# Kernel tuning notes

Hardware: AMD Instinct MI355X
Metric: run time of the kernel (lower is better)

The kernel has to match this reference:

```python
import jax, jax.numpy as jnp
import numpy as np

B, S, D = 16, 2048, 1024
FF = 4 * D
ST, EN = 0, 512          # target_dims['start'], target_dims['end']
DT = EN - ST             # intervened subspace dim


def setup_inputs() -> dict:
    key = jax.random.key(0)
    k = jax.random.split(key, 6)
    hidden_states = jax.random.normal(k[0], (B, S, D), dtype=jnp.float32)
    eot_indices = jax.random.randint(k[1], (B,), 0, S)
    scale = 0.02
    W1 = jax.random.normal(k[2], (D, FF), dtype=jnp.float32) * scale
    W2 = jax.random.normal(k[3], (FF, D), dtype=jnp.float32) * scale
    W_rot = jax.random.normal(k[4], (DT, DT), dtype=jnp.float32) * scale
    W_inv = jax.random.normal(k[5], (DT, DT), dtype=jnp.float32) * scale
    return {"hidden_states": hidden_states, "W1": W1, "W2": W2,
            "W_rot": W_rot, "W_inv": W_inv, "eot_indices": eot_indices}


def reference(hidden_states, W1, W2, W_rot, W_inv, eot_indices):
    # layers[0]: transformer FFN block (stand-in for the wrapped encoder layer)
    h = jax.nn.gelu(hidden_states @ W1) @ W2          # [B, S, D]
    b = jnp.arange(h.shape[0])
    # LinearLayer branch: gather per-example eot row, slice target subspace
    rows = h[b, eot_indices]                          # [B, D]
    target = rows[:, ST:EN]                           # [B, DT]
    # LinearLayer -> InverseLinearLayer: rotate then un-rotate the subspace
    intervention = (target @ W_rot) @ W_inv           # [B, DT]
    # scatter/replace back into the flattened hidden states (vectorized form
    # of the per-example flatten/slice/cat/stack loop in the original code)
    new_rows = rows.at[:, ST:EN].set(intervention)    # [B, D]
    reps = h.at[b, eot_indices].set(new_rows)         # [B, S, D]
    return reps
```

## Files before the change

kernel.cpp:

```cpp
#include <hip/hip_runtime.h>
#include <hip/hip_bf16.h>
#include <stdint.h>

#define B_SZ  16
#define S_SZ  2048
#define D_SZ  1024
#define FF_SZ 4096
#define DT_SZ 512

typedef __bf16 bf16x8 __attribute__((ext_vector_type(8)));
typedef float  f32x4  __attribute__((ext_vector_type(4)));
typedef short  short8 __attribute__((ext_vector_type(8)));

__device__ __forceinline__ short f2bf(float x) {
    union { float f; uint32_t u; } v; v.f = x;
    uint32_t r = (v.u + 0x7fffu + ((v.u >> 16) & 1u)) >> 16;
    return (short)(uint16_t)r;
}

__global__ void cast_x_kernel(const float* __restrict__ src, short* __restrict__ dst, int n8) {
    int i = blockIdx.x * 256 + threadIdx.x;
    if (i >= n8) return;
    const float4* s4 = reinterpret_cast<const float4*>(src);
    float4 a = s4[2 * i], b = s4[2 * i + 1];
    short8 v;
    v[0] = f2bf(a.x); v[1] = f2bf(a.y); v[2] = f2bf(a.z); v[3] = f2bf(a.w);
    v[4] = f2bf(b.x); v[5] = f2bf(b.y); v[6] = f2bf(b.z); v[7] = f2bf(b.w);
    reinterpret_cast<short8*>(dst)[i] = v;
}

__global__ void transpose_cast_kernel(const float* __restrict__ src, short* __restrict__ dst,
                                      int R, int C) {
    __shared__ float tile[32][33];
    int c0 = blockIdx.x * 32, r0 = blockIdx.y * 32;
    int tx = threadIdx.x, ty = threadIdx.y;
#pragma unroll
    for (int i = 0; i < 32; i += 8)
        tile[ty + i][tx] = src[(size_t)(r0 + ty + i) * C + (c0 + tx)];
    __syncthreads();
#pragma unroll
    for (int i = 0; i < 32; i += 8)
        dst[(size_t)(c0 + ty + i) * R + (r0 + tx)] = f2bf(tile[tx][ty + i]);
}


#define GLOAD(srcp, dstofs)                                                   \
    __builtin_amdgcn_global_load_lds(                                         \
        (__attribute__((address_space(1))) void*)(srcp),                      \
        (__attribute__((address_space(3))) void*)(ldsb + (dstofs)), 16, 0, 0)

#define ABASE(S) ((S) * 65536)
#define BBASE(S) ((S) * 65536 + 32768)

#define STG_A(S, H, T) do {                                                                 \
    GLOAD(gA[H][0] + (size_t)(T) * 64, ABASE(S) + (H) * 16384 +        w * 1024);           \
    GLOAD(gA[H][1] + (size_t)(T) * 64, ABASE(S) + (H) * 16384 + 8192 + w * 1024);           \
} while (0)
#define STG_B(S, H, T) do {                                                                 \
    GLOAD(gB[H][0] + (size_t)(T) * 64, BBASE(S) + (H) * 16384 +        w * 1024);           \
    GLOAD(gB[H][1] + (size_t)(T) * 64, BBASE(S) + (H) * 16384 + 8192 + w * 1024);           \
} while (0)
#define NOSTG ((void)0)
#define VM2  asm volatile("s_waitcnt vmcnt(2)" ::: "memory")
#define VM0  asm volatile("s_waitcnt vmcnt(0)" ::: "memory")
#define NOVM ((void)0)

#define PHASE(S, KS, MIG, RB, VM, ...) do {                                                 \
    if (RB) {                                                                               \
        _Pragma("unroll")                                                                   \
        for (int ni = 0; ni < 4; ++ni)                                                      \
            bfv[ni] = *reinterpret_cast<const bf16x8*>(                                     \
                ldsb + BBASE(S) + (offB[ni] ^ ((KS) * 64)));                                \
    }                                                                                       \
    _Pragma("unroll")                                                                       \
    for (int mi = 0; mi < 4; ++mi)                                                          \
        af[mi] = *reinterpret_cast<const bf16x8*>(                                          \
            ldsb + ABASE(S) + (offA[(MIG) * 4 + mi] ^ ((KS) * 64)));                        \
    __VA_ARGS__;                                                                            \
    __builtin_amdgcn_s_barrier();                                                           \
    asm volatile("s_waitcnt lgkmcnt(0)" ::: "memory");                                      \
    __builtin_amdgcn_sched_barrier(0);                                                      \
    __builtin_amdgcn_s_setprio(1);                                                          \
    _Pragma("unroll")                                                                       \
    for (int mi = 0; mi < 4; ++mi)                                                          \
        _Pragma("unroll")                                                                   \
        for (int ni = 0; ni < 4; ++ni)                                                      \
            acc[(MIG) * 4 + mi][ni] = __builtin_amdgcn_mfma_f32_16x16x32_bf16(              \
                af[mi], bfv[ni], acc[(MIG) * 4 + mi][ni], 0, 0, 0);                         \
    __builtin_amdgcn_s_setprio(0);                                                          \
    __builtin_amdgcn_sched_barrier(0);                                                      \
    VM;                                                                                     \
    __builtin_amdgcn_s_barrier();                                                           \
} while (0)

#define ITER_FULL(T) do {                                                                   \
    PHASE(0, 0, 0, 1, NOVM, STG_B(1, 1, (T) + 1));                                          \
    PHASE(0, 0, 1, 0, NOVM, STG_A(1, 0, (T) + 1));                                          \
    PHASE(0, 1, 0, 1, NOVM, STG_A(1, 1, (T) + 1));                                          \
    PHASE(0, 1, 1, 0, VM2,  STG_B(0, 0, (T) + 2));                                          \
    PHASE(1, 0, 0, 1, NOVM, STG_B(0, 1, (T) + 2));                                          \
    PHASE(1, 0, 1, 0, NOVM, STG_A(0, 0, (T) + 2));                                          \
    PHASE(1, 1, 0, 1, NOVM, STG_A(0, 1, (T) + 2));                                          \
    PHASE(1, 1, 1, 0, VM2,  STG_B(1, 0, (T) + 3));                                          \
} while (0)

#define ITER_LAST(T) do {                                                                   \
    PHASE(0, 0, 0, 1, NOVM, STG_B(1, 1, (T) + 1));                                          \
    PHASE(0, 0, 1, 0, NOVM, STG_A(1, 0, (T) + 1));                                          \
    PHASE(0, 1, 0, 1, NOVM, STG_A(1, 1, (T) + 1));                                          \
    PHASE(0, 1, 1, 0, VM0,  NOSTG);                                                         \
    PHASE(1, 0, 0, 1, NOVM, NOSTG);                                                         \
    PHASE(1, 0, 1, 0, NOVM, NOSTG);                                                         \
    PHASE(1, 1, 0, 1, NOVM, NOSTG);                                                         \
    PHASE(1, 1, 1, 0, NOVM, NOSTG);                                                         \
} while (0)

template <bool GELU_BF16>
__global__ __launch_bounds__(512, 2)
void gemm256_kernel(const short* __restrict__ A, const short* __restrict__ Bt,
                    void* __restrict__ Cout, int M, int N, int K) {
    __shared__ char lds2[2][65536];
    char* ldsb = &lds2[0][0];

    const int tid = threadIdx.x;
    const int w   = tid >> 6;
    const int l   = tid & 63;
    const int wm  = w >> 2;
    const int wn  = w & 3;
    const int kq  = l >> 4;
    const int l15 = l & 15;

    const int nwg = gridDim.x;
    int swzw = blockIdx.x;
    if ((nwg & 7) == 0) swzw = (swzw & 7) * (nwg >> 3) + (swzw >> 3);
    const int MB = M >> 8;
    const int bm = swzw % MB, bn = swzw / MB;
    const int m0 = bm << 8, n0 = bn << 8;

    int offA[8], offB[4];
#pragma unroll
    for (int mi = 0; mi < 8; ++mi) {
        const int r = wm * 128 + mi * 16 + l15;
        offA[mi] = r * 128 + ((kq ^ (r & 7)) << 4);
    }
#pragma unroll
    for (int ni = 0; ni < 4; ++ni) {
        const int r = wn * 64 + ni * 16 + l15;
        offB[ni] = r * 128 + ((kq ^ (r & 7)) << 4);
    }

    const short *gA[2][2], *gB[2][2];
#pragma unroll
    for (int h = 0; h < 2; ++h)
#pragma unroll
        for (int j = 0; j < 2; ++j) {
            const int X = tid * 16 + j * 8192;
            const int P = X ^ (((X >> 7) & 7) << 4);
            const int r = P >> 7, c = (P & 127) >> 1;
            gA[h][j] = A  + (size_t)(m0 + h * 128 + r) * K + c;
            gB[h][j] = Bt + (size_t)(n0 + h * 128 + r) * K + c;
        }

    f32x4 acc[8][4];
#pragma unroll
    for (int mi = 0; mi < 8; ++mi)
#pragma unroll
        for (int ni = 0; ni < 4; ++ni)
            acc[mi][ni] = (f32x4){0.f, 0.f, 0.f, 0.f};

    bf16x8 af[4], bfv[4];
    const int NT = K >> 6;
    const int NI = NT >> 1;

    STG_B(0, 0, 0);
    STG_B(0, 1, 0);
    STG_A(0, 0, 0);
    STG_A(0, 1, 0);
    STG_B(1, 0, 1);
    VM2;
    __builtin_amdgcn_s_barrier();

    for (int i = 0; i < NI - 1; ++i) {
        const int T = 2 * i;
        ITER_FULL(T);
    }
    ITER_LAST(2 * (NI - 1));

    const int row_base = m0 + wm * 128 + kq * 4;
    const int col_base = n0 + wn * 64 + l15;
    if constexpr (GELU_BF16) {
        short* C = reinterpret_cast<short*>(Cout);
#pragma unroll
        for (int mi = 0; mi < 8; ++mi)
#pragma unroll
            for (int r = 0; r < 4; ++r) {
                const size_t ro = (size_t)(row_base + mi * 16 + r) * N;
#pragma unroll
                for (int ni = 0; ni < 4; ++ni) {
                    float x = acc[mi][ni][r];
                    float u = 0.7978845608028654f * (x + 0.044715f * x * x * x);
                    float g = x / (1.f + __expf(-2.f * u));
                    C[ro + col_base + ni * 16] = f2bf(g);
                }
            }
    } else {
        float* C = reinterpret_cast<float*>(Cout);
#pragma unroll
        for (int mi = 0; mi < 8; ++mi)
#pragma unroll
            for (int r = 0; r < 4; ++r) {
                const size_t ro = (size_t)(row_base + mi * 16 + r) * N;
#pragma unroll
                for (int ni = 0; ni < 4; ++ni)
                    C[ro + col_base + ni * 16] = acc[mi][ni][r];
            }
    }
}

__global__ void intervention_kernel(const float* __restrict__ Wrot, const float* __restrict__ Winv,
                                    const int* __restrict__ eot, float* __restrict__ out) {
    __shared__ float tgt[DT_SZ];
    __shared__ float tmp[DT_SZ];
    const int b = blockIdx.x;
    const int j = threadIdx.x;
    float* row = out + ((size_t)b * S_SZ + eot[b]) * D_SZ;
    tgt[j] = row[j];
    __syncthreads();
    float s = 0.f;
#pragma unroll 8
    for (int i = 0; i < DT_SZ; ++i) s = fmaf(tgt[i], Wrot[(size_t)i * DT_SZ + j], s);
    tmp[j] = s;
    __syncthreads();
    float s2 = 0.f;
#pragma unroll 8
    for (int i = 0; i < DT_SZ; ++i) s2 = fmaf(tmp[i], Winv[(size_t)i * DT_SZ + j], s2);
    row[j] = s2;
}

extern "C" void kernel_launch(void* const* d_in, const int* in_sizes, int n_in,
                              void* d_out, int out_size, void* d_ws, size_t ws_size,
                              hipStream_t stream) {
    const float* hidden = (const float*)d_in[0];
    const float* W1     = (const float*)d_in[1];
    const float* W2     = (const float*)d_in[2];
    const float* Wrot   = (const float*)d_in[3];
    const float* Winv   = (const float*)d_in[4];
    const int*   eot    = (const int*)d_in[5];
    float* out = (float*)d_out;

    const int M = B_SZ * S_SZ;

    short* W1t = (short*)d_ws;
    short* W2t = W1t + (size_t)FF_SZ * D_SZ;
    short* Xbf = W2t + (size_t)FF_SZ * D_SZ;
    const size_t fixed_bytes = 2ull * (size_t)FF_SZ * D_SZ * sizeof(short);
    const size_t per_row = (size_t)D_SZ * 2 + (size_t)FF_SZ * 2;
    size_t rem = ws_size > fixed_bytes ? ws_size - fixed_bytes : 0;
    int Mc = (int)(rem / per_row);
    Mc = (Mc / 512) * 512;
    if (Mc < 512) Mc = 512;
    if (Mc > M) Mc = M;
    short* C1 = Xbf + (size_t)Mc * D_SZ;

    transpose_cast_kernel<<<dim3(FF_SZ / 32, D_SZ / 32), dim3(32, 8), 0, stream>>>(W1, W1t, D_SZ, FF_SZ);
    transpose_cast_kernel<<<dim3(D_SZ / 32, FF_SZ / 32), dim3(32, 8), 0, stream>>>(W2, W2t, FF_SZ, D_SZ);

    for (int ms = 0; ms < M; ms += Mc) {
        const int mc = (M - ms < Mc) ? (M - ms) : Mc;
        const int n8 = mc * D_SZ / 8;
        cast_x_kernel<<<(n8 + 255) / 256, 256, 0, stream>>>(hidden + (size_t)ms * D_SZ, Xbf, n8);
        gemm256_kernel<true ><<<dim3((mc / 256) * (FF_SZ / 256)), 512, 0, stream>>>(
            Xbf, W1t, C1, mc, FF_SZ, D_SZ);
        gemm256_kernel<false><<<dim3((mc / 256) * (D_SZ / 256)), 512, 0, stream>>>(
            C1, W2t, out + (size_t)ms * D_SZ, mc, D_SZ, FF_SZ);
    }
    intervention_kernel<<<B_SZ, DT_SZ, 0, stream>>>(Wrot, Winv, eot, out);
}
```

Baseline: 672.4 us.

## Double-buffer LDS fragment registers to overlap ds_reads with MFMA

Restructures the 256x256 GEMM main loop so the LDS reads for the next phase are issued into a second register set (af0/af1, bf0/bf1) while the MFMAs of the current phase run. This removes the per-phase lgkmcnt(0) wait before compute, and the global-to-LDS staging and vmcnt waits are rescheduled to fit. It uses more VGPRs, which could cause spills under launch_bounds(512,2), and it relies on the barrier placement to keep buffer reuse safe.

```diff
diff --git a/kernel.cpp b/kernel.cpp
--- a/kernel.cpp
+++ b/kernel.cpp
@@ -60,59 +60,77 @@
     GLOAD(gB[H][0] + (size_t)(T) * 64, BBASE(S) + (H) * 16384 +        w * 1024);           \
     GLOAD(gB[H][1] + (size_t)(T) * 64, BBASE(S) + (H) * 16384 + 8192 + w * 1024);           \
 } while (0)
-#define NOSTG ((void)0)
+
+#define VM4  asm volatile("s_waitcnt vmcnt(4)" ::: "memory")
 #define VM2  asm volatile("s_waitcnt vmcnt(2)" ::: "memory")
 #define VM0  asm volatile("s_waitcnt vmcnt(0)" ::: "memory")
-#define NOVM ((void)0)
-
-#define PHASE(S, KS, MIG, RB, VM, ...) do {                                                 \
-    if (RB) {                                                                               \
-        _Pragma("unroll")                                                                   \
-        for (int ni = 0; ni < 4; ++ni)                                                      \
-            bfv[ni] = *reinterpret_cast<const bf16x8*>(                                     \
-                ldsb + BBASE(S) + (offB[ni] ^ ((KS) * 64)));                                \
-    }                                                                                       \
+
+#define READ_A(dst, S, KS, MIG) do {                                                        \
     _Pragma("unroll")                                                                       \
     for (int mi = 0; mi < 4; ++mi)                                                          \
-        af[mi] = *reinterpret_cast<const bf16x8*>(                                          \
+        dst[mi] = *reinterpret_cast<const bf16x8*>(                                         \
             ldsb + ABASE(S) + (offA[(MIG) * 4 + mi] ^ ((KS) * 64)));                        \
-    __VA_ARGS__;                                                                            \
-    __builtin_amdgcn_s_barrier();                                                           \
-    asm volatile("s_waitcnt lgkmcnt(0)" ::: "memory");                                      \
-    __builtin_amdgcn_sched_barrier(0);                                                      \
+} while (0)
+#define READ_B(dst, S, KS) do {                                                             \
+    _Pragma("unroll")                                                                       \
+    for (int ni = 0; ni < 4; ++ni)                                                          \
+        dst[ni] = *reinterpret_cast<const bf16x8*>(                                         \
+            ldsb + BBASE(S) + (offB[ni] ^ ((KS) * 64)));                                    \
+} while (0)
+
+#define MFMA16(AF, BF, MIG) do {                                                            \
     __builtin_amdgcn_s_setprio(1);                                                          \
     _Pragma("unroll")                                                                       \
     for (int mi = 0; mi < 4; ++mi)                                                          \
         _Pragma("unroll")                                                                   \
         for (int ni = 0; ni < 4; ++ni)                                                      \
             acc[(MIG) * 4 + mi][ni] = __builtin_amdgcn_mfma_f32_16x16x32_bf16(              \
-                af[mi], bfv[ni], acc[(MIG) * 4 + mi][ni], 0, 0, 0);                         \
+                AF[mi], BF[ni], acc[(MIG) * 4 + mi][ni], 0, 0, 0);                          \
     __builtin_amdgcn_s_setprio(0);                                                          \
+} while (0)
+
+#define BAR() do {                                                                          \
     __builtin_amdgcn_sched_barrier(0);                                                      \
-    VM;                                                                                     \
     __builtin_amdgcn_s_barrier();                                                           \
 } while (0)
+#define SB() __builtin_amdgcn_sched_barrier(0)
 
 #define ITER_FULL(T) do {                                                                   \
-    PHASE(0, 0, 0, 1, NOVM, STG_B(1, 1, (T) + 1));                                          \
-    PHASE(0, 0, 1, 0, NOVM, STG_A(1, 0, (T) + 1));                                          \
-    PHASE(0, 1, 0, 1, NOVM, STG_A(1, 1, (T) + 1));                                          \
-    PHASE(0, 1, 1, 0, VM2,  STG_B(0, 0, (T) + 2));                                          \
-    PHASE(1, 0, 0, 1, NOVM, STG_B(0, 1, (T) + 2));                                          \
-    PHASE(1, 0, 1, 0, NOVM, STG_A(0, 0, (T) + 2));                                          \
-    PHASE(1, 1, 0, 1, NOVM, STG_A(0, 1, (T) + 2));                                          \
-    PHASE(1, 1, 1, 0, VM2,  STG_B(1, 0, (T) + 3));                                          \
+     STG_B(1, 1, (T) + 1);                     BAR();                               \
+             READ_A(af1, 0, 0, 1);                     SB(); MFMA16(af0, bf0, 0);           \
+     STG_A(1, 0, (T) + 1); STG_A(1, 1, (T) + 1); BAR();                             \
+             READ_A(af0, 0, 1, 0); READ_B(bf1, 0, 1);  SB(); MFMA16(af1, bf0, 1);           \
+                                               BAR();                               \
+             READ_A(af1, 0, 1, 1);                     SB(); MFMA16(af0, bf1, 0);           \
+     STG_B(0, 0, (T) + 2); STG_B(0, 1, (T) + 2); VM4; BAR();                        \
+             READ_A(af0, 1, 0, 0); READ_B(bf0, 1, 0);  SB(); MFMA16(af1, bf1, 1);           \
+     STG_A(0, 0, (T) + 2); STG_A(0, 1, (T) + 2); BAR();                             \
+             READ_A(af1, 1, 0, 1);                     SB(); MFMA16(af0, bf0, 0);           \
+                                               BAR();                               \
+             READ_A(af0, 1, 1, 0); READ_B(bf1, 1, 1);  SB(); MFMA16(af1, bf0, 1);           \
+                                               BAR();                               \
+             READ_A(af1, 1, 1, 1);                     SB(); MFMA16(af0, bf1, 0);           \
+     STG_B(1, 0, (T) + 3); VM2;                BAR();                               \
+             READ_A(af0, 0, 0, 0); READ_B(bf0, 0, 0);  SB(); MFMA16(af1, bf1, 1);           \
 } while (0)
 
 #define ITER_LAST(T) do {                                                                   \
-    PHASE(0, 0, 0, 1, NOVM, STG_B(1, 1, (T) + 1));                                          \
-    PHASE(0, 0, 1, 0, NOVM, STG_A(1, 0, (T) + 1));                                          \
-    PHASE(0, 1, 0, 1, NOVM, STG_A(1, 1, (T) + 1));                                          \
-    PHASE(0, 1, 1, 0, VM0,  NOSTG);                                                         \
-    PHASE(1, 0, 0, 1, NOVM, NOSTG);                                                         \
-    PHASE(1, 0, 1, 0, NOVM, NOSTG);                                                         \
-    PHASE(1, 1, 0, 1, NOVM, NOSTG);                                                         \
-    PHASE(1, 1, 1, 0, NOVM, NOSTG);                                                         \
+     STG_B(1, 1, (T) + 1);                     BAR();                               \
+             READ_A(af1, 0, 0, 1);                     SB(); MFMA16(af0, bf0, 0);           \
+     STG_A(1, 0, (T) + 1); STG_A(1, 1, (T) + 1); BAR();                             \
+             READ_A(af0, 0, 1, 0); READ_B(bf1, 0, 1);  SB(); MFMA16(af1, bf0, 1);           \
+                                               BAR();                               \
+             READ_A(af1, 0, 1, 1);                     SB(); MFMA16(af0, bf1, 0);           \
+     VM0;                                      BAR();                               \
+             READ_A(af0, 1, 0, 0); READ_B(bf0, 1, 0);  SB(); MFMA16(af1, bf1, 1);           \
+                                               BAR();                               \
+             READ_A(af1, 1, 0, 1);                     SB(); MFMA16(af0, bf0, 0);           \
+                                               BAR();                               \
+             READ_A(af0, 1, 1, 0); READ_B(bf1, 1, 1);  SB(); MFMA16(af1, bf0, 1);           \
+                                               BAR();                               \
+             READ_A(af1, 1, 1, 1);                     SB(); MFMA16(af0, bf1, 0);           \
+                                               BAR();                               \
+             SB(); MFMA16(af1, bf1, 1);                                                     \
 } while (0)
 
 template <bool GELU_BF16>
@@ -168,7 +186,7 @@
         for (int ni = 0; ni < 4; ++ni)
             acc[mi][ni] = (f32x4){0.f, 0.f, 0.f, 0.f};
 
-    bf16x8 af[4], bfv[4];
+    bf16x8 af0[4], af1[4], bf0[4], bf1[4];
     const int NT = K >> 6;
     const int NI = NT >> 1;
 
@@ -178,13 +196,14 @@
     STG_A(0, 1, 0);
     STG_B(1, 0, 1);
     VM2;
-    __builtin_amdgcn_s_barrier();
-
-    for (int i = 0; i < NI - 1; ++i) {
-        const int T = 2 * i;
-        ITER_FULL(T);
-    }
-    ITER_LAST(2 * (NI - 1));
+    BAR();
+    READ_A(af0, 0, 0, 0);
+    READ_B(bf0, 0, 0);
+    SB();
+
+    for (int i = 0; i < NI - 1; ++i)
+        ITER_FULL(2 * i);
+    ITER_LAST(NT - 2);
 
     const int row_base = m0 + wm * 128 + kq * 4;
     const int col_base = n0 + wn * 64 + l15;
```

Result: slower. 729.8 us (+8.5%).
